# Kernel tuning notes

Measured on AMD Instinct MI355X. Metric: run time of the kernel, lower is better.

## Reference

```python
import jax, jax.numpy as jnp
import numpy as np

B, CIN, COUT, H, W = 4, 256, 256, 64, 64
K, G = 3, 4
PAD = (K - 1) // 2


def setup_inputs() -> dict:
    key = jax.random.key(0)
    k0, k1, k2, k3 = jax.random.split(key, 4)
    x = jax.random.normal(k0, (B, CIN, H, W), jnp.float32)
    y = jax.random.normal(k1, (B, 2, H, W), jnp.float32)
    # conv_offset: 1x1 conv, no bias, init std=0.1 (normal_init)
    w_offset = jax.random.normal(k2, (G * 2 * K * K, 2, 1, 1), jnp.float32) * 0.1
    # DeformConv2d weight, no bias, init std=0.01
    w_deform = jax.random.normal(k3, (COUT, CIN, K, K), jnp.float32) * 0.01
    return {"x": x, "y": y, "w_offset": w_offset, "w_deform": w_deform}


def _deform_conv(x, offset, weight):
    """DCN v1: stride 1, dilation 1, zero padding PAD, deform_groups=G, groups=1."""
    KK = K * K
    # mmcv offset layout: [B, G*2*KK, H, W] -> per group, per kernel pos, (dy, dx)
    off = offset.reshape(B, G, KK, 2, H, W)
    dy, dx = off[:, :, :, 0], off[:, :, :, 1]            # [B,G,KK,H,W]
    ii, jj = jnp.meshgrid(jnp.arange(K), jnp.arange(K), indexing="ij")
    ky = ii.reshape(KK).astype(x.dtype)                  # kernel row offsets
    kx = jj.reshape(KK).astype(x.dtype)                  # kernel col offsets
    base_y = jnp.arange(H, dtype=x.dtype)[None, :, None] - PAD + ky[:, None, None]  # [KK,H,1]
    base_x = jnp.arange(W, dtype=x.dtype)[None, None, :] - PAD + kx[:, None, None]  # [KK,1,W]
    yc = dy + base_y                                     # [B,G,KK,H,W]
    xc = dx + base_x

    Cg = CIN // G
    xg = x.reshape(B, G, Cg, H, W)

    def sample(xg1, yc1, xc1):
        # xg1 [Cg,H,W]; yc1/xc1 [KK,H,W] -> bilinear sample with zero padding
        y0 = jnp.floor(yc1)
        x0 = jnp.floor(xc1)
        wy = yc1 - y0
        wx = xc1 - x0
        y0i = y0.astype(jnp.int32)
        x0i = x0.astype(jnp.int32)

        def gather(yi, xi):
            valid = (yi >= 0) & (yi < H) & (xi >= 0) & (xi < W)
            v = xg1[:, jnp.clip(yi, 0, H - 1), jnp.clip(xi, 0, W - 1)]  # [Cg,KK,H,W]
            return v * valid[None].astype(xg1.dtype)

        v00 = gather(y0i, x0i)
        v01 = gather(y0i, x0i + 1)
        v10 = gather(y0i + 1, x0i)
        v11 = gather(y0i + 1, x0i + 1)
        return (v00 * (1 - wy) * (1 - wx) + v01 * (1 - wy) * wx
                + v10 * wy * (1 - wx) + v11 * wy * wx)

    sampled = jax.vmap(jax.vmap(sample))(xg, yc, xc)     # [B,G,Cg,KK,H,W]
    sampled = sampled.reshape(B, CIN, KK, H, W)
    wflat = weight.reshape(COUT, CIN, KK)
    return jnp.einsum("bckhw,ock->bohw", sampled, wflat)  # [B,COUT,H,W]


def reference(x, y, w_offset, w_deform):
    # offset = conv_offset(y.detach()), a 1x1 conv without bias
    y_det = jax.lax.stop_gradient(y)
    offset = jnp.einsum("bihw,oi->bohw", y_det, w_offset[:, :, 0, 0])
    out = _deform_conv(x, offset, w_deform)
    return jax.nn.relu(out)
```

## Files before the change

kernel.cpp:

```cpp
#include <hip/hip_runtime.h>
#include <cstddef>

#define B_    4
#define CIN_  256
#define COUT_ 256
#define H_    64
#define W_    64
#define KK_   9
#define G_    4
#define PW    80
#define PH    80
#define PADO  8

typedef short bf16x8 __attribute__((ext_vector_type(8)));
typedef float f32x4  __attribute__((ext_vector_type(4)));
typedef __attribute__((address_space(1))) const unsigned int* gptr_t;
typedef __attribute__((address_space(3))) unsigned int*       lptr_t;

__device__ __forceinline__ unsigned short f2bf(float v) {
    unsigned int u = __float_as_uint(v);
    u += 0x7fffu + ((u >> 16) & 1u);
    return (unsigned short)(u >> 16);
}
__device__ __forceinline__ float f_lo(unsigned int u) { return __uint_as_float(u << 16); }
__device__ __forceinline__ float f_hi(unsigned int u) { return __uint_as_float(u & 0xffff0000u); }

__global__ __launch_bounds__(256) void prep_kernel(const float* __restrict__ x,
                                                   unsigned short* __restrict__ xTp,
                                                   const float* __restrict__ w,
                                                   unsigned short* __restrict__ wb) {
    const int tid = threadIdx.x;
    if (blockIdx.x < 512) {
        __shared__ unsigned short s[128][66];
        const int bh    = blockIdx.x >> 1;
        const int chalf = blockIdx.x & 1;
        const int b     = bh >> 6, h = bh & 63;
        const size_t src_base = ((size_t)b * CIN_ + chalf * 128) * (H_ * W_) + h * W_;
        #pragma unroll 4
        for (int k = 0; k < 32; ++k) {
            int i = k * 256 + tid;
            int c = i >> 6, ww = i & 63;
            s[c][ww] = f2bf(x[src_base + (size_t)c * (H_ * W_) + ww]);
        }
        __syncthreads();
        const size_t dst_row = ((size_t)b * PH + (h + PADO)) * PW;
        #pragma unroll 4
        for (int k = 0; k < 20; ++k) {
            int j  = k * 256 + tid;
            int c2 = (j & 63) * 2, wp = j >> 6;
            unsigned int v = 0;
            if (wp >= PADO && wp < PADO + W_) {
                int ww = wp - PADO;
                v = (unsigned int)s[c2][ww] | ((unsigned int)s[c2 + 1][ww] << 16);
            }
            *(unsigned int*)(xTp + (dst_row + wp) * 256 + chalf * 128 + c2) = v;
        }
    } else if (blockIdx.x < 576) {
        const int bidx = blockIdx.x - 512;
        const int b = bidx >> 4, rr = bidx & 15;
        const int yp = (rr < PADO) ? rr : (PH - 16 + rr);
        unsigned short* dst = xTp + ((size_t)b * PH + yp) * PW * 256;
        #pragma unroll
        for (int k = 0; k < 10; ++k) {
            *(uint4*)(dst + (size_t)(k * 256 + tid) * 8) = make_uint4(0, 0, 0, 0);
        }
    } else {
        int idx = (blockIdx.x - 576) * 256 + tid;
        int e   = idx & 7;
        int pos = (idx >> 3) & 7;
        int o   = (idx >> 6) & 255;
        int t   = idx >> 14;
        int g   = t / 9, kk = t - g * 9;
        int j   = pos ^ (o & 7);
        int c   = g * 64 + j * 8 + e;
        wb[idx] = f2bf(w[(o * CIN_ + c) * KK_ + kk]);
    }
}

__global__ __launch_bounds__(512, 2) void dcn_kernel(
    const unsigned short* __restrict__ xTp, const float* __restrict__ y,
    const float* __restrict__ w_off, const unsigned short* __restrict__ wb,
    float* __restrict__ out)
{
    __shared__ unsigned short s_W[2][2][16384];
    __shared__ unsigned short s_S[2][2][4096];

    const int tid = threadIdx.x;
    const int bid = blockIdx.x;
    const int xcd = bid & 7;
    const int b   = xcd >> 1;
    const int h   = (xcd & 1) * 32 + (bid >> 3);

    const int sp = tid >> 3;
    const int c8 = tid & 7;

    const float yv0 = y[((b * 2 + 0) * H_ + h) * W_ + sp];
    const float yv1 = y[((b * 2 + 1) * H_ + h) * W_ + sp];
    const float spf = (float)(sp - 1 + PADO);
    const float hpf = (float)(h  - 1 + PADO);

    const int lane = tid & 63, wave = tid >> 6;
    const int pg  = wave & 1, oh = wave >> 1;
    const int l15 = lane & 15, kq = lane >> 4, sw = l15 & 7;

    f32x4 acc[8];
    #pragma unroll
    for (int i = 0; i < 8; ++i) acc[i] = (f32x4){0.f, 0.f, 0.f, 0.f};

    const unsigned short* xb = xTp + (size_t)b * (PH * PW * 256) + c8 * 8;

    float wgt[2][4];
    uint4 gA[2], gB[2], gC[2], gD[2];

#define ISSUE_ONE(t, P) do {                                                   \
    const int t_ = (t);                                                        \
    const int g_ = t_ / 9, kk_ = t_ - g_ * 9;                                  \
    const float4 co = *(const float4*)(w_off + t_ * 4);                        \
    const float dy = fmaf(yv0, co.x, yv1 * co.y);                              \
    const float dx = fmaf(yv0, co.z, yv1 * co.w);                              \
    const float yc = hpf + (float)(kk_ / 3) + dy;                              \
    const float xc = spf + (float)(kk_ % 3) + dx;                              \
    const float yf = floorf(yc), xf = floorf(xc);                              \
    const float wy = yc - yf, wx = xc - xf;                                    \
    const int   yi = (int)yf, xi = (int)xf;           \
    const float omy = 1.f - wy, omx = 1.f - wx;                                \
    wgt[P][0] = omy * omx; wgt[P][1] = omy * wx;                               \
    wgt[P][2] = wy * omx;  wgt[P][3] = wy * wx;                                \
    const unsigned short* p0 = xb + (yi * PW + xi) * 256 + g_ * 64;            \
    const unsigned short* p1 = p0 + PW * 256;                                  \
    gA[P] = *(const uint4*)(p0);        gB[P] = *(const uint4*)(p0 + 256);     \
    gC[P] = *(const uint4*)(p1);        gD[P] = *(const uint4*)(p1 + 256);     \
} while (0)

#define STAGE_W2(t, buf) do {                                                  \
    const unsigned short* src = wb + (size_t)(t) * 32768;                      \
    _Pragma("unroll")                                                          \
    for (int j = 0; j < 8; ++j) {                                              \
        const int off = (j * 512 + tid) * 8;                                   \
        __builtin_amdgcn_global_load_lds((gptr_t)(src + off),                  \
                                         (lptr_t)(&s_W[buf][0][0] + off),      \
                                         16, 0, 0);                            \
    }                                                                          \
} while (0)

#define WRITE_ONE(P, SB) do {                                                  \
    const unsigned int av[4] = {gA[P].x, gA[P].y, gA[P].z, gA[P].w};           \
    const unsigned int bv[4] = {gB[P].x, gB[P].y, gB[P].z, gB[P].w};           \
    const unsigned int cv[4] = {gC[P].x, gC[P].y, gC[P].z, gC[P].w};           \
    const unsigned int dv[4] = {gD[P].x, gD[P].y, gD[P].z, gD[P].w};           \
    unsigned int res[4];                                                       \
    _Pragma("unroll")                                                          \
    for (int q = 0; q < 4; ++q) {                                              \
        float rl = wgt[P][0] * f_lo(av[q]);                                    \
        rl = fmaf(wgt[P][1], f_lo(bv[q]), rl);                                 \
        rl = fmaf(wgt[P][2], f_lo(cv[q]), rl);                                 \
        rl = fmaf(wgt[P][3], f_lo(dv[q]), rl);                                 \
        float rh = wgt[P][0] * f_hi(av[q]);                                    \
        rh = fmaf(wgt[P][1], f_hi(bv[q]), rh);                                 \
        rh = fmaf(wgt[P][2], f_hi(cv[q]), rh);                                 \
        rh = fmaf(wgt[P][3], f_hi(dv[q]), rh);                                 \
        res[q] = __builtin_amdgcn_perm(__float_as_uint(rh),                    \
                                       __float_as_uint(rl), 0x07060302u);      \
    }                                                                          \
    *(uint4*)(&s_S[SB][P][0] + sp * 64 + ((c8 ^ (sp & 7)) * 8)) =              \
        make_uint4(res[0], res[1], res[2], res[3]);                            \
} while (0)

#define MFMA_TAP(WB, HF, SB) do {                                              \
    bf16x8 bf[2][2], af[2][4];                                                 \
    _Pragma("unroll")                                                          \
    for (int kh = 0; kh < 2; ++kh) {                                           \
        const int pos = ((kh * 4 + kq) ^ sw) * 8;                              \
        _Pragma("unroll")                                                      \
        for (int nt = 0; nt < 2; ++nt)                                         \
            bf[kh][nt] = *(const bf16x8*)(&s_S[SB][HF][0] +                    \
                              (pg * 32 + nt * 16 + l15) * 64 + pos);           \
        _Pragma("unroll")                                                      \
        for (int mt = 0; mt < 4; ++mt)                                         \
            af[kh][mt] = *(const bf16x8*)(&s_W[WB][HF][0] +                    \
                              (oh * 64 + mt * 16 + l15) * 64 + pos);           \
    }                                                                          \
    __builtin_amdgcn_s_setprio(1);                                             \
    _Pragma("unroll")                                                          \
    for (int kh = 0; kh < 2; ++kh)                                             \
        _Pragma("unroll")                                                      \
        for (int nt = 0; nt < 2; ++nt)                                         \
            _Pragma("unroll")                                                  \
            for (int mt = 0; mt < 4; ++mt)                                     \
                acc[nt * 4 + mt] = __builtin_amdgcn_mfma_f32_16x16x32_bf16(    \
                    af[kh][mt], bf[kh][nt], acc[nt * 4 + mt], 0, 0, 0);        \
    __builtin_amdgcn_s_setprio(0);                                             \
} while (0)

#define STEP(s_, P, DO_PF) do {                                                \
    if (DO_PF) { ISSUE_ONE(2 * (s_) + 2, 0); ISSUE_ONE(2 * (s_) + 3, 1); }     \
    if (DO_PF) STAGE_W2((s_) + 1, P ^ 1);                                      \
    MFMA_TAP(P, 0, P);                                                         \
    if (DO_PF) WRITE_ONE(0, P ^ 1);                                            \
    MFMA_TAP(P, 1, P);                                                         \
    if (DO_PF) WRITE_ONE(1, P ^ 1);                                            \
    __syncthreads();                                                           \
} while (0)

    ISSUE_ONE(0, 0);
    ISSUE_ONE(1, 1);
    STAGE_W2(0, 0);
    WRITE_ONE(0, 0);
    WRITE_ONE(1, 0);
    __syncthreads();

    for (int sb = 0; sb < 16; sb += 2) {
        STEP(sb + 0, 0, 1);
        STEP(sb + 1, 1, 1);
    }
    STEP(16, 0, 1);
    MFMA_TAP(1, 0, 1);
    MFMA_TAP(1, 1, 1);

    #pragma unroll
    for (int nt = 0; nt < 2; ++nt) {
        const int px = pg * 32 + nt * 16 + l15;
        #pragma unroll
        for (int mt = 0; mt < 4; ++mt) {
            const int obase = oh * 64 + mt * 16 + kq * 4;
            #pragma unroll
            for (int rr = 0; rr < 4; ++rr) {
                out[(((size_t)b * COUT_ + obase + rr) * H_ + h) * W_ + px] =
                    fmaxf(acc[nt * 4 + mt][rr], 0.f);
            }
        }
    }
#undef ISSUE_ONE
#undef STAGE_W2
#undef WRITE_ONE
#undef MFMA_TAP
#undef STEP
}

extern "C" void kernel_launch(void* const* d_in, const int* in_sizes, int n_in,
                              void* d_out, int out_size, void* d_ws, size_t ws_size,
                              hipStream_t stream) {
    const float* x     = (const float*)d_in[0];
    const float* y     = (const float*)d_in[1];
    const float* w_off = (const float*)d_in[2];
    const float* w_def = (const float*)d_in[3];
    float* out = (float*)d_out;

    unsigned short* xTp = (unsigned short*)d_ws;
    unsigned short* wb  = (unsigned short*)d_ws + (size_t)B_ * PH * PW * 256;

    prep_kernel<<<2880, 256, 0, stream>>>(x, xTp, w_def, wb);
    dcn_kernel<<<256, 512, 0, stream>>>(xTp, y, w_off, wb, out);
}
```

Baseline: 117.8 us.

## Split output channels across two blocks and pipeline one tap per stage

The DCN kernel now launches twice as many blocks, each computing half of the output channels (128) for one row. Each pipeline stage now handles a single tap-group slice instead of two, which shrinks LDS buffers and accumulator registers so occupancy can rise (launch bounds of 4 blocks). The cost is that the bilinear sampling work is duplicated across the two channel halves, and there are twice as many barriers per block.

```diff
diff --git a/kernel.cpp b/kernel.cpp
--- a/kernel.cpp
+++ b/kernel.cpp
@@ -8,6 +8,7 @@
 #define W_    64
 #define KK_   9
 #define G_    4
+#define NSL   36
 #define PW    80
 #define PH    80
 #define PADO  8
@@ -77,19 +78,21 @@
     }
 }
 
-__global__ __launch_bounds__(512, 2) void dcn_kernel(
+__global__ __launch_bounds__(512, 4) void dcn_kernel(
     const unsigned short* __restrict__ xTp, const float* __restrict__ y,
     const float* __restrict__ w_off, const unsigned short* __restrict__ wb,
     float* __restrict__ out)
 {
-    __shared__ unsigned short s_W[2][2][16384];
-    __shared__ unsigned short s_S[2][2][4096];
+    __shared__ unsigned short s_W[2][128 * 64];
+    __shared__ unsigned short s_S[2][64 * 64];
 
     const int tid = threadIdx.x;
     const int bid = blockIdx.x;
-    const int xcd = bid & 7;
-    const int b   = xcd >> 1;
-    const int h   = (xcd & 1) * 32 + (bid >> 3);
+    const int ohalf = bid >> 8;
+    const int r     = bid & 255;
+    const int xcd   = r & 7;
+    const int b     = xcd >> 1;
+    const int h     = (xcd & 1) * 32 + (r >> 3);
 
     const int sp = tid >> 3;
     const int c8 = tid & 7;
@@ -103,16 +106,16 @@
     const int pg  = wave & 1, oh = wave >> 1;
     const int l15 = lane & 15, kq = lane >> 4, sw = l15 & 7;
 
-    f32x4 acc[8];
+    f32x4 acc[4];
     #pragma unroll
-    for (int i = 0; i < 8; ++i) acc[i] = (f32x4){0.f, 0.f, 0.f, 0.f};
+    for (int i = 0; i < 4; ++i) acc[i] = (f32x4){0.f, 0.f, 0.f, 0.f};
 
     const unsigned short* xb = xTp + (size_t)b * (PH * PW * 256) + c8 * 8;
 
-    float wgt[2][4];
-    uint4 gA[2], gB[2], gC[2], gD[2];
-
-#define ISSUE_ONE(t, P) do {                                                   \
+    float wgt[4];
+    uint4 gA, gB, gC, gD;
+
+#define ISSUE_ONE(t) do {                                                      \
     const int t_ = (t);                                                        \
     const int g_ = t_ / 9, kk_ = t_ - g_ * 9;                                  \
     const float4 co = *(const float4*)(w_off + t_ * 4);                        \
@@ -124,61 +127,61 @@
     const float wy = yc - yf, wx = xc - xf;                                    \
     const int   yi = (int)yf, xi = (int)xf;           \
     const float omy = 1.f - wy, omx = 1.f - wx;                                \
-    wgt[P][0] = omy * omx; wgt[P][1] = omy * wx;                               \
-    wgt[P][2] = wy * omx;  wgt[P][3] = wy * wx;                                \
+    wgt[0] = omy * omx; wgt[1] = omy * wx;                                     \
+    wgt[2] = wy * omx;  wgt[3] = wy * wx;                                      \
     const unsigned short* p0 = xb + (yi * PW + xi) * 256 + g_ * 64;            \
     const unsigned short* p1 = p0 + PW * 256;                                  \
-    gA[P] = *(const uint4*)(p0);        gB[P] = *(const uint4*)(p0 + 256);     \
-    gC[P] = *(const uint4*)(p1);        gD[P] = *(const uint4*)(p1 + 256);     \
-} while (0)
-
-#define STAGE_W2(t, buf) do {                                                  \
-    const unsigned short* src = wb + (size_t)(t) * 32768;                      \
-    _Pragma("unroll")                                                          \
-    for (int j = 0; j < 8; ++j) {                                              \
+    gA = *(const uint4*)(p0);        gB = *(const uint4*)(p0 + 256);           \
+    gC = *(const uint4*)(p1);        gD = *(const uint4*)(p1 + 256);           \
+} while (0)
+
+#define STAGE_W(t, buf) do {                                                   \
+    const unsigned short* src = wb + (size_t)(t) * 16384 + ohalf * 8192;       \
+    _Pragma("unroll")                                                          \
+    for (int j = 0; j < 2; ++j) {                                              \
         const int off = (j * 512 + tid) * 8;                                   \
         __builtin_amdgcn_global_load_lds((gptr_t)(src + off),                  \
-                                         (lptr_t)(&s_W[buf][0][0] + off),      \
+                                         (lptr_t)(&s_W[buf][0] + off),         \
                                          16, 0, 0);                            \
     }                                                                          \
 } while (0)
 
-#define WRITE_ONE(P, SB) do {                                                  \
-    const unsigned int av[4] = {gA[P].x, gA[P].y, gA[P].z, gA[P].w};           \
-    const unsigned int bv[4] = {gB[P].x, gB[P].y, gB[P].z, gB[P].w};           \
-    const unsigned int cv[4] = {gC[P].x, gC[P].y, gC[P].z, gC[P].w};           \
-    const unsigned int dv[4] = {gD[P].x, gD[P].y, gD[P].z, gD[P].w};           \
+#define WRITE_ONE(SB) do {                                                     \
+    const unsigned int av[4] = {gA.x, gA.y, gA.z, gA.w};                       \
+    const unsigned int bv[4] = {gB.x, gB.y, gB.z, gB.w};                       \
+    const unsigned int cv[4] = {gC.x, gC.y, gC.z, gC.w};                       \
+    const unsigned int dv[4] = {gD.x, gD.y, gD.z, gD.w};                       \
     unsigned int res[4];                                                       \
     _Pragma("unroll")                                                          \
     for (int q = 0; q < 4; ++q) {                                              \
-        float rl = wgt[P][0] * f_lo(av[q]);                                    \
-        rl = fmaf(wgt[P][1], f_lo(bv[q]), rl);                                 \
-        rl = fmaf(wgt[P][2], f_lo(cv[q]), rl);                                 \
-        rl = fmaf(wgt[P][3], f_lo(dv[q]), rl);                                 \
-        float rh = wgt[P][0] * f_hi(av[q]);                                    \
-        rh = fmaf(wgt[P][1], f_hi(bv[q]), rh);                                 \
-        rh = fmaf(wgt[P][2], f_hi(cv[q]), rh);                                 \
-        rh = fmaf(wgt[P][3], f_hi(dv[q]), rh);                                 \
+        float rl = wgt[0] * f_lo(av[q]);                                       \
+        rl = fmaf(wgt[1], f_lo(bv[q]), rl);                                    \
+        rl = fmaf(wgt[2], f_lo(cv[q]), rl);                                    \
+        rl = fmaf(wgt[3], f_lo(dv[q]), rl);                                    \
+        float rh = wgt[0] * f_hi(av[q]);                                       \
+        rh = fmaf(wgt[1], f_hi(bv[q]), rh);                                    \
+        rh = fmaf(wgt[2], f_hi(cv[q]), rh);                                    \
+        rh = fmaf(wgt[3], f_hi(dv[q]), rh);                                    \
         res[q] = __builtin_amdgcn_perm(__float_as_uint(rh),                    \
                                        __float_as_uint(rl), 0x07060302u);      \
     }                                                                          \
-    *(uint4*)(&s_S[SB][P][0] + sp * 64 + ((c8 ^ (sp & 7)) * 8)) =              \
+    *(uint4*)(&s_S[SB][0] + sp * 64 + ((c8 ^ (sp & 7)) * 8)) =                 \
         make_uint4(res[0], res[1], res[2], res[3]);                            \
 } while (0)
 
-#define MFMA_TAP(WB, HF, SB) do {                                              \
-    bf16x8 bf[2][2], af[2][4];                                                 \
+#define MFMA_TAP(WB, SB) do {                                                  \
+    bf16x8 bf[2][2], af[2][2];                                                 \
     _Pragma("unroll")                                                          \
     for (int kh = 0; kh < 2; ++kh) {                                           \
         const int pos = ((kh * 4 + kq) ^ sw) * 8;                              \
         _Pragma("unroll")                                                      \
         for (int nt = 0; nt < 2; ++nt)                                         \
-            bf[kh][nt] = *(const bf16x8*)(&s_S[SB][HF][0] +                    \
+            bf[kh][nt] = *(const bf16x8*)(&s_S[SB][0] +                        \
                               (pg * 32 + nt * 16 + l15) * 64 + pos);           \
         _Pragma("unroll")                                                      \
-        for (int mt = 0; mt < 4; ++mt)                                         \
-            af[kh][mt] = *(const bf16x8*)(&s_W[WB][HF][0] +                    \
-                              (oh * 64 + mt * 16 + l15) * 64 + pos);           \
+        for (int mt = 0; mt < 2; ++mt)                                         \
+            af[kh][mt] = *(const bf16x8*)(&s_W[WB][0] +                        \
+                              (oh * 32 + mt * 16 + l15) * 64 + pos);           \
     }                                                                          \
     __builtin_amdgcn_s_setprio(1);                                             \
     _Pragma("unroll")                                                          \
@@ -186,55 +189,54 @@
         _Pragma("unroll")                                                      \
         for (int nt = 0; nt < 2; ++nt)                                         \
             _Pragma("unroll")                                                  \
-            for (int mt = 0; mt < 4; ++mt)                                     \
-                acc[nt * 4 + mt] = __builtin_amdgcn_mfma_f32_16x16x32_bf16(    \
-                    af[kh][mt], bf[kh][nt], acc[nt * 4 + mt], 0, 0, 0);        \
+            for (int mt = 0; mt < 2; ++mt)                                     \
+                acc[nt * 2 + mt] = __builtin_amdgcn_mfma_f32_16x16x32_bf16(    \
+                    af[kh][mt], bf[kh][nt], acc[nt * 2 + mt], 0, 0, 0);        \
     __builtin_amdgcn_s_setprio(0);                                             \
 } while (0)
 
-#define STEP(s_, P, DO_PF) do {                                                \
-    if (DO_PF) { ISSUE_ONE(2 * (s_) + 2, 0); ISSUE_ONE(2 * (s_) + 3, 1); }     \
-    if (DO_PF) STAGE_W2((s_) + 1, P ^ 1);                                      \
-    MFMA_TAP(P, 0, P);                                                         \
-    if (DO_PF) WRITE_ONE(0, P ^ 1);                                            \
-    MFMA_TAP(P, 1, P);                                                         \
-    if (DO_PF) WRITE_ONE(1, P ^ 1);                                            \
-    __syncthreads();                                                           \
-} while (0)
-
-    ISSUE_ONE(0, 0);
-    ISSUE_ONE(1, 1);
-    STAGE_W2(0, 0);
-    WRITE_ONE(0, 0);
-    WRITE_ONE(1, 0);
+    ISSUE_ONE(0);
+    STAGE_W(0, 0);
+    WRITE_ONE(0);
     __syncthreads();
 
-    for (int sb = 0; sb < 16; sb += 2) {
-        STEP(sb + 0, 0, 1);
-        STEP(sb + 1, 1, 1);
+    for (int t = 0; t < 34; t += 2) {
+        ISSUE_ONE(t + 1);
+        STAGE_W(t + 1, 1);
+        MFMA_TAP(0, 0);
+        WRITE_ONE(1);
+        __syncthreads();
+
+        ISSUE_ONE(t + 2);
+        STAGE_W(t + 2, 0);
+        MFMA_TAP(1, 1);
+        WRITE_ONE(0);
+        __syncthreads();
     }
-    STEP(16, 0, 1);
-    MFMA_TAP(1, 0, 1);
-    MFMA_TAP(1, 1, 1);
+    ISSUE_ONE(35);
+    STAGE_W(35, 1);
+    MFMA_TAP(0, 0);
+    WRITE_ONE(1);
+    __syncthreads();
+    MFMA_TAP(1, 1);
 
     #pragma unroll
     for (int nt = 0; nt < 2; ++nt) {
         const int px = pg * 32 + nt * 16 + l15;
         #pragma unroll
-        for (int mt = 0; mt < 4; ++mt) {
-            const int obase = oh * 64 + mt * 16 + kq * 4;
+        for (int mt = 0; mt < 2; ++mt) {
+            const int obase = ohalf * 128 + oh * 32 + mt * 16 + kq * 4;
             #pragma unroll
             for (int rr = 0; rr < 4; ++rr) {
                 out[(((size_t)b * COUT_ + obase + rr) * H_ + h) * W_ + px] =
-                    fmaxf(acc[nt * 4 + mt][rr], 0.f);
+                    fmaxf(acc[nt * 2 + mt][rr], 0.f);
             }
         }
     }
 #undef ISSUE_ONE
-#undef STAGE_W2
+#undef STAGE_W
 #undef WRITE_ONE
 #undef MFMA_TAP
-#undef STEP
 }
 
 extern "C" void kernel_launch(void* const* d_in, const int* in_sizes, int n_in,
@@ -250,5 +252,5 @@
     unsigned short* wb  = (unsigned short*)d_ws + (size_t)B_ * PH * PW * 256;
 
     prep_kernel<<<2880, 256, 0, stream>>>(x, xTp, w_def, wb);
-    dcn_kernel<<<256, 512, 0, stream>>>(xTp, y, w_off, wb, out);
-}
+    dcn_kernel<<<512, 512, 0, stream>>>(xTp, y, w_off, wb, out);
+}
```

Measured after the change: 119.8 us. No clear change (+1.7%).
